# Optimization experiments

Hardware: AMD Instinct MI355X
Metric: run time of the kernel (lower is better)

## Reference

```python
import jax, jax.numpy as jnp
import numpy as np

SPALIZED_CHANNELS = 50


def setup_inputs() -> dict:
    key = jax.random.key(0)
    k_img, k_mask = jax.random.split(key)
    img = jax.random.normal(k_img, (3, 512, 512), dtype=jnp.float32)
    mask = jax.random.randint(k_mask, (512, 512), 0, SPALIZED_CHANNELS, dtype=jnp.int64)
    return {"img": img, "mask": mask}


def reference(img, mask):
    # One-hot route each pixel's channels to the output slot given by its mask label.
    # obj ids: [K,1,1,1]; mask: [1,1,H,W] -> onehot [K,1,H,W]; img [1,C,H,W]
    obj_ids = jnp.arange(SPALIZED_CHANNELS, dtype=mask.dtype)[:, None, None, None]
    onehot = (mask[None, None, :, :] == obj_ids).astype(img.dtype)  # [K,1,H,W]
    spalized_img = img[None, :, :, :] * onehot  # [K,C,H,W]
    return (spalized_img, mask)
```

## Files before the change

kernel.cpp:

```cpp
#include <hip/hip_runtime.h>
#include <hip/hip_bf16.h>


#define K  50
#define C  3
#define H  512
#define W  512
#define HW (H * W)
#define PIX_PER_THREAD 4
#define NTHREADS (HW / PIX_PER_THREAD)

__global__ __launch_bounds__(256) void spalize_kernel(
    const float* __restrict__ img,
    const int*   __restrict__ mask,
    float*       __restrict__ out)
{
    const int tid = blockIdx.x * blockDim.x + threadIdx.x;
    const int p = tid * PIX_PER_THREAD;

    const int4 m = *reinterpret_cast<const int4*>(mask + p);

    float4 mf;
    mf.x = (float)m.x; mf.y = (float)m.y; mf.z = (float)m.z; mf.w = (float)m.w;
    *reinterpret_cast<float4*>(out + (size_t)K * C * HW + p) = mf;

    const float4 a0 = *reinterpret_cast<const float4*>(img + 0 * HW + p);
    const float4 a1 = *reinterpret_cast<const float4*>(img + 1 * HW + p);
    const float4 a2 = *reinterpret_cast<const float4*>(img + 2 * HW + p);

    float* base = out + p;

#pragma unroll
    for (int k = 0; k < K; ++k) {
        float4 o0, o1, o2;
        o0.x = (m.x == k) ? a0.x : 0.0f;
        o0.y = (m.y == k) ? a0.y : 0.0f;
        o0.z = (m.z == k) ? a0.z : 0.0f;
        o0.w = (m.w == k) ? a0.w : 0.0f;

        o1.x = (m.x == k) ? a1.x : 0.0f;
        o1.y = (m.y == k) ? a1.y : 0.0f;
        o1.z = (m.z == k) ? a1.z : 0.0f;
        o1.w = (m.w == k) ? a1.w : 0.0f;

        o2.x = (m.x == k) ? a2.x : 0.0f;
        o2.y = (m.y == k) ? a2.y : 0.0f;
        o2.z = (m.z == k) ? a2.z : 0.0f;
        o2.w = (m.w == k) ? a2.w : 0.0f;

        *reinterpret_cast<float4*>(base + ((size_t)(k * C + 0)) * HW) = o0;
        *reinterpret_cast<float4*>(base + ((size_t)(k * C + 1)) * HW) = o1;
        *reinterpret_cast<float4*>(base + ((size_t)(k * C + 2)) * HW) = o2;
    }
}

extern "C" void kernel_launch(void* const* d_in, const int* in_sizes, int n_in,
                              void* d_out, int out_size, void* d_ws, size_t ws_size,
                              hipStream_t stream) {
    const float* img  = (const float*)d_in[0];
    const int*   mask = (const int*)d_in[1];
    float*       out  = (float*)d_out;

    const int block = 256;
    const int grid  = NTHREADS / block;
    spalize_kernel<<<grid, block, 0, stream>>>(img, mask, out);
}
```

Measured before the change: 157.5 us.

## Parallelize over output elements instead of looping all channels per pixel

Each thread now produces one float4 of the output, working out its plane (k, c) and pixel from a flat index, rather than one thread writing all 150 planes for four pixels. This gives far more threads and fully contiguous stores across a wavefront, so the write stream that dominates the kernel can be spread across more of the GPU. The cost is that mask and img are re-read once per output plane, though those reads should mostly hit in cache.

```diff
diff --git a/kernel.cpp b/kernel.cpp
--- a/kernel.cpp
+++ b/kernel.cpp
@@ -7,50 +7,40 @@
 #define H  512
 #define W  512
 #define HW (H * W)
-#define PIX_PER_THREAD 4
-#define NTHREADS (HW / PIX_PER_THREAD)
+#define OUT0 (K * C * HW)
+#define OUT_TOTAL (OUT0 + HW)
+#define BLOCK 256
 
-__global__ __launch_bounds__(256) void spalize_kernel(
+__global__ __launch_bounds__(BLOCK) void spalize_kernel(
     const float* __restrict__ img,
     const int*   __restrict__ mask,
     float*       __restrict__ out)
 {
-    const int tid = blockIdx.x * blockDim.x + threadIdx.x;
-    const int p = tid * PIX_PER_THREAD;
+    const int tid = blockIdx.x * BLOCK + threadIdx.x;
+    const int f = tid * 4;
 
-    const int4 m = *reinterpret_cast<const int4*>(mask + p);
+    if (f < OUT0) {
+        const int plane = f >> 18;
+        const int p     = f & (HW - 1);
+        const int k     = (plane * 0x5556) >> 16;
+        const int c     = plane - k * 3;
 
-    float4 mf;
-    mf.x = (float)m.x; mf.y = (float)m.y; mf.z = (float)m.z; mf.w = (float)m.w;
-    *reinterpret_cast<float4*>(out + (size_t)K * C * HW + p) = mf;
+        const int4   m = *reinterpret_cast<const int4*>(mask + p);
+        const float4 a = *reinterpret_cast<const float4*>(img + c * HW + p);
 
-    const float4 a0 = *reinterpret_cast<const float4*>(img + 0 * HW + p);
-    const float4 a1 = *reinterpret_cast<const float4*>(img + 1 * HW + p);
-    const float4 a2 = *reinterpret_cast<const float4*>(img + 2 * HW + p);
-
-    float* base = out + p;
-
-#pragma unroll
-    for (int k = 0; k < K; ++k) {
-        float4 o0, o1, o2;
-        o0.x = (m.x == k) ? a0.x : 0.0f;
-        o0.y = (m.y == k) ? a0.y : 0.0f;
-        o0.z = (m.z == k) ? a0.z : 0.0f;
-        o0.w = (m.w == k) ? a0.w : 0.0f;
-
-        o1.x = (m.x == k) ? a1.x : 0.0f;
-        o1.y = (m.y == k) ? a1.y : 0.0f;
-        o1.z = (m.z == k) ? a1.z : 0.0f;
-        o1.w = (m.w == k) ? a1.w : 0.0f;
-
-        o2.x = (m.x == k) ? a2.x : 0.0f;
-        o2.y = (m.y == k) ? a2.y : 0.0f;
-        o2.z = (m.z == k) ? a2.z : 0.0f;
-        o2.w = (m.w == k) ? a2.w : 0.0f;
-
-        *reinterpret_cast<float4*>(base + ((size_t)(k * C + 0)) * HW) = o0;
-        *reinterpret_cast<float4*>(base + ((size_t)(k * C + 1)) * HW) = o1;
-        *reinterpret_cast<float4*>(base + ((size_t)(k * C + 2)) * HW) = o2;
+        float4 o;
+        o.x = (m.x == k) ? a.x : 0.0f;
+        o.y = (m.y == k) ? a.y : 0.0f;
+        o.z = (m.z == k) ? a.z : 0.0f;
+        o.w = (m.w == k) ? a.w : 0.0f;
+        *reinterpret_cast<float4*>(out + f) = o;
+    } else {
+        const int p = f - OUT0;
+        const int4 m = *reinterpret_cast<const int4*>(mask + p);
+        float4 mf;
+        mf.x = (float)m.x; mf.y = (float)m.y;
+        mf.z = (float)m.z; mf.w = (float)m.w;
+        *reinterpret_cast<float4*>(out + f) = mf;
     }
 }
 
@@ -61,7 +51,7 @@
     const int*   mask = (const int*)d_in[1];
     float*       out  = (float*)d_out;
 
-    const int block = 256;
-    const int grid  = NTHREADS / block;
-    spalize_kernel<<<grid, block, 0, stream>>>(img, mask, out);
+    const int nthreads = OUT_TOTAL / 4;
+    const int grid = nthreads / BLOCK;
+    spalize_kernel<<<grid, BLOCK, 0, stream>>>(img, mask, out);
 }
```

New measurement: 156.7 us (median of 2 runs). Within noise of the previous version (-0.5%).
